# Performance work log

Hardware: AMD Instinct MI355X
Metric: run time of the kernel (lower is better)

Reference implementation:

```python
import jax, jax.numpy as jnp
import numpy as np

N = 2048          # num nodes
C = 256           # dense_dim per input
EMB = 3 * C       # 768
H = 8             # num_heads
D = EMB // H      # 96 head_dim
ALPHA = 0.2       # leaky relu slope
SCALE = D ** -0.5


def setup_inputs() -> dict:
    key = jax.random.key(0)
    ks = jax.random.split(key, 9)
    sd = EMB ** -0.5
    return {
        "eh": jax.random.normal(ks[0], (N, C), jnp.float32),
        "er": jax.random.normal(ks[1], (N, C), jnp.float32),
        "et": jax.random.normal(ks[2], (N, C), jnp.float32),
        "h_id": jax.random.randint(ks[3], (N,), 0, 32),
        "W_w": jax.random.normal(ks[4], (EMB, EMB), jnp.float32) * sd,
        "a": jax.random.normal(ks[5], (2 * D, 1), jnp.float32) * (2 * D) ** -0.5,
        "proj_w": jax.random.normal(ks[6], (EMB, EMB), jnp.float32) * sd,
        "proj_b": jnp.zeros((EMB,), jnp.float32),
        "skip_w": jax.random.normal(ks[7], (EMB, EMB), jnp.float32) * sd,
        "skip_b": jnp.zeros((EMB,), jnp.float32),
    }


def reference(eh, er, et, h_id, W_w, a, proj_w, proj_b, skip_w, skip_b):
    n = eh.shape[0]
    e = jnp.concatenate([eh, er, et], axis=-1)            # [N, EMB]
    Wh = (e @ W_w.T).reshape(n, H, D)                     # [N, H, D]

    # score = leakyrelu(a1 . Wh_scrambled[i] + a2 . Wh[j]) * scale
    a1, a2 = a[:D, 0], a[D:, 0]
    s1 = Wh @ a1                                          # [N, H]
    s2 = Wh @ a2                                          # [N, H]
    # torch's Wh.repeat(1,1,N).view(N*N,H,D) reads head (j*H + h)//N for pair (i,j,h)
    qidx = (jnp.arange(n)[:, None] * H + jnp.arange(H)[None, :]) // n  # [N, H]
    x = s1[:, qidx] + s2[None, :, :]                      # [N, N, H]
    e_ij = jnp.where(x >= 0, x, ALPHA * x) * SCALE

    mask = h_id[:, None] != h_id[None, :]                 # [N, N]
    e_ij = jnp.where(mask[:, :, None], -jnp.inf, e_ij)
    attn = jax.nn.softmax(e_ij, axis=1)                   # softmax over neighbors j

    out = jnp.einsum('ijh,jhd->ihd', attn, Wh).reshape(n, H * D)
    out = out @ proj_w.T + proj_b                         # [N, EMB]
    skip = e @ skip_w.T + skip_b                          # [N, EMB]
    return skip + out
```

## Files before the change

kernel.cpp:

```cpp
#include <hip/hip_runtime.h>
#include <hip/hip_bf16.h>

#define N_NODES 2048
#define EMB 768
#define NH 8
#define DH 96
#define ALPHA 0.2f
#define SCALE 0.10206207261596575f
#define NGMAX 192
#define WSZ (EMB * EMB)

typedef __bf16 bf16x8 __attribute__((ext_vector_type(8)));
typedef float f32x4 __attribute__((ext_vector_type(4)));
typedef __attribute__((address_space(3))) unsigned int lds_u32;
typedef __attribute__((address_space(1))) const unsigned int glb_u32;

union pack4 { ushort4 u; __hip_bfloat16 h[4]; };

__global__ __launch_bounds__(256) void prep_kernel(
    const float* __restrict__ eh, const float* __restrict__ er, const float* __restrict__ et,
    const float* __restrict__ W0, const float* __restrict__ W1, const float* __restrict__ W2,
    __hip_bfloat16* __restrict__ e, __hip_bfloat16* __restrict__ o0,
    __hip_bfloat16* __restrict__ o1, __hip_bfloat16* __restrict__ o2, int* __restrict__ cnt)
{
    const int b = blockIdx.x;
    const int gtid = b * 256 + threadIdx.x;
    if (gtid < 32) cnt[gtid] = 0;
    const float* src;
    __hip_bfloat16* dst;
    if (b < 1536) {
        int idx = gtid * 4;
        int i = idx / EMB, c = idx % EMB;
        if (c < 256)      src = eh + i * 256 + c;
        else if (c < 512) src = er + i * 256 + (c - 256);
        else              src = et + i * 256 + (c - 512);
        dst = e + (size_t)i * EMB + c;
    } else {
        int idx = (gtid - 1536 * 256) * 4;
        if (idx < WSZ)          { src = W0 + idx;           dst = o0 + idx; }
        else if (idx < 2 * WSZ) { src = W1 + idx - WSZ;     dst = o1 + idx - WSZ; }
        else                    { src = W2 + idx - 2 * WSZ; dst = o2 + idx - 2 * WSZ; }
    }
    float4 v = *reinterpret_cast<const float4*>(src);
    pack4 p;
    p.h[0] = __float2bfloat16(v.x);
    p.h[1] = __float2bfloat16(v.y);
    p.h[2] = __float2bfloat16(v.z);
    p.h[3] = __float2bfloat16(v.w);
    *reinterpret_cast<ushort4*>(dst) = p.u;
}

__device__ __forceinline__ void stage128(
    const __hip_bfloat16* __restrict__ src, int row0, int k0,
    __hip_bfloat16* lds, int wave, int lane)
{
#pragma unroll
    for (int i = 0; i < 4; i++) {
        const int c0 = wave * 256 + i * 64;
        const int c = c0 + lane;
        const int row = c >> 4;
        const int cb = (c & 15) ^ (row & 15);
        const __hip_bfloat16* g = src + (size_t)(row0 + row) * EMB + k0 + cb * 8;
        __builtin_amdgcn_global_load_lds((glb_u32*)g, (lds_u32*)(lds + c0 * 8), 16, 0, 0);
    }
}

__global__ __launch_bounds__(256) void gemm_nt_kernel(
    const __hip_bfloat16* __restrict__ A1, const __hip_bfloat16* __restrict__ B1, int ns1,
    const __hip_bfloat16* __restrict__ A2, const __hip_bfloat16* __restrict__ B2, int ns2,
    const float* __restrict__ bias1, const float* __restrict__ bias2,
    float* __restrict__ Cf)
{
    __shared__ __attribute__((aligned(16))) __hip_bfloat16 sm[2][2][8192];

    const int t = threadIdx.x;
    const int lane = t & 63, wave = t >> 6;
    const int wm = wave >> 1, wn = wave & 1;
    const int bm = blockIdx.y * 64, bn = blockIdx.x * 64;
    const int l15 = lane & 15, quad = lane >> 4;
    const int NS = ns1 + ns2;
    const int rA = wm * 32 + l15, rB = wn * 32 + l15;

    f32x4 acc00 = {0.f,0.f,0.f,0.f}, acc01 = {0.f,0.f,0.f,0.f};
    f32x4 acc10 = {0.f,0.f,0.f,0.f}, acc11 = {0.f,0.f,0.f,0.f};

    stage128(A1, bm, 0, &sm[0][0][0], wave, lane);
    stage128(B1, bn, 0, &sm[0][1][0], wave, lane);

    for (int s = 0; s < NS; s++) {
        __syncthreads();
        if (s + 1 < NS) {
            const int sn = s + 1;
            const __hip_bfloat16* As = (sn < ns1) ? A1 : A2;
            const __hip_bfloat16* Bs = (sn < ns1) ? B1 : B2;
            const int k0 = ((sn < ns1) ? sn : sn - ns1) * 128;
            stage128(As, bm, k0, &sm[sn & 1][0][0], wave, lane);
            stage128(Bs, bn, k0, &sm[sn & 1][1][0], wave, lane);
        }
        const __hip_bfloat16* At = &sm[s & 1][0][0];
        const __hip_bfloat16* Bt = &sm[s & 1][1][0];
#pragma unroll
        for (int ks = 0; ks < 4; ks++) {
            const int cq = ks * 4 + quad;
            bf16x8 a0 = *(const bf16x8*)(At + (size_t)(rA * 16        + (cq ^ l15)) * 8);
            bf16x8 a1 = *(const bf16x8*)(At + (size_t)((rA + 16) * 16 + (cq ^ l15)) * 8);
            bf16x8 b0 = *(const bf16x8*)(Bt + (size_t)(rB * 16        + (cq ^ l15)) * 8);
            bf16x8 b1 = *(const bf16x8*)(Bt + (size_t)((rB + 16) * 16 + (cq ^ l15)) * 8);
            acc00 = __builtin_amdgcn_mfma_f32_16x16x32_bf16(a0, b0, acc00, 0, 0, 0);
            acc01 = __builtin_amdgcn_mfma_f32_16x16x32_bf16(a0, b1, acc01, 0, 0, 0);
            acc10 = __builtin_amdgcn_mfma_f32_16x16x32_bf16(a1, b0, acc10, 0, 0, 0);
            acc11 = __builtin_amdgcn_mfma_f32_16x16x32_bf16(a1, b1, acc11, 0, 0, 0);
        }
    }

    const int col0 = bn + wn * 32 + l15;
    const int col1 = col0 + 16;
    float bv0 = 0.f, bv1 = 0.f;
    if (bias1 != nullptr) {
        bv0 = bias1[col0] + bias2[col0];
        bv1 = bias1[col1] + bias2[col1];
    }
    const int r0 = bm + wm * 32 + quad * 4;
#pragma unroll
    for (int r = 0; r < 4; r++) {
        const int row0 = r0 + r, row1 = r0 + 16 + r;
        Cf[(size_t)row0 * EMB + col0] = acc00[r] + bv0;
        Cf[(size_t)row0 * EMB + col1] = acc01[r] + bv1;
        Cf[(size_t)row1 * EMB + col0] = acc10[r] + bv0;
        Cf[(size_t)row1 * EMB + col1] = acc11[r] + bv1;
    }
}

__global__ __launch_bounds__(256) void s12g_kernel(
    const float* __restrict__ Wh, const float* __restrict__ a,
    float* __restrict__ s1, float* __restrict__ s2,
    const int* __restrict__ h_id, int* __restrict__ cnt, int* __restrict__ lists)
{
    int gid = blockIdx.x * 256 + threadIdx.x;
    if (gid < N_NODES) {
        int g = h_id[gid];
        int p = atomicAdd(&cnt[g], 1);
        lists[g * N_NODES + p] = gid;
    }
    int i = gid >> 3, h = gid & 7;
    const float* wr = Wh + (size_t)i * EMB + h * DH;
    float acc1 = 0.f, acc2 = 0.f;
    for (int d = 0; d < DH; d++) {
        float w = wr[d];
        acc1 += w * a[d];
        acc2 += w * a[DH + d];
    }
    s1[gid] = acc1;
    s2[gid] = acc2;
}

__global__ __launch_bounds__(256) void attn_kernel(
    const float* __restrict__ Wh, const float* __restrict__ s1, const float* __restrict__ s2,
    const int* __restrict__ cnt, const int* __restrict__ lists,
    __hip_bfloat16* __restrict__ out)
{
    const int g  = blockIdx.x & 31;
    const int h  = (blockIdx.x >> 5) & 7;
    const int dh = blockIdx.x >> 8;
    const int t  = threadIdx.x;

    __shared__ int   jb[NGMAX];
    __shared__ int   qg[NGMAX];
    __shared__ float s2g[NGMAX];
    __shared__ float s1g[NGMAX][9];
    __shared__ float Whg[NGMAX][48];

    const int ng = min(cnt[g], NGMAX);
    const int* gl = lists + g * N_NODES;

    for (int j = t; j < ng; j += 256) {
        int node = gl[j];
        jb[j]  = node;
        qg[j]  = node >> 8;
        s2g[j] = s2[node * 8 + h];
        float4 v0 = *reinterpret_cast<const float4*>(s1 + node * 8);
        float4 v1 = *reinterpret_cast<const float4*>(s1 + node * 8 + 4);
        s1g[j][0] = v0.x; s1g[j][1] = v0.y; s1g[j][2] = v0.z; s1g[j][3] = v0.w;
        s1g[j][4] = v1.x; s1g[j][5] = v1.y; s1g[j][6] = v1.z; s1g[j][7] = v1.w;
    }
    __syncthreads();
    for (int idx = t; idx < ng * 12; idx += 256) {
        int jc = idx / 12, dq = idx % 12;
        float4 v = *reinterpret_cast<const float4*>(
            Wh + (size_t)jb[jc] * EMB + h * DH + dh * 48 + dq * 4);
        *reinterpret_cast<float4*>(&Whg[jc][dq * 4]) = v;
    }
    __syncthreads();

    if (t < ng) {
        float m = -1e30f;
        for (int j = 0; j < ng; j++) {
            float x = s1g[t][qg[j]] + s2g[j];
            float ev = (x >= 0.f ? x : ALPHA * x) * SCALE;
            m = fmaxf(m, ev);
        }
        float S = 0.f;
        for (int j = 0; j < ng; j++) {
            float x = s1g[t][qg[j]] + s2g[j];
            float ev = (x >= 0.f ? x : ALPHA * x) * SCALE;
            S += __expf(ev - m);
        }
        const float ri = 1.f / S;

        float acc[48];
#pragma unroll
        for (int d = 0; d < 48; d++) acc[d] = 0.f;
        for (int j = 0; j < ng; j++) {
            float x = s1g[t][qg[j]] + s2g[j];
            float ev = (x >= 0.f ? x : ALPHA * x) * SCALE;
            float p = __expf(ev - m) * ri;
#pragma unroll
            for (int d = 0; d < 48; d++) acc[d] += p * Whg[j][d];
        }
        __hip_bfloat16* po = out + (size_t)jb[t] * EMB + h * DH + dh * 48;
#pragma unroll
        for (int d = 0; d < 48; d += 4) {
            pack4 pk;
            pk.h[0] = __float2bfloat16(acc[d]);
            pk.h[1] = __float2bfloat16(acc[d + 1]);
            pk.h[2] = __float2bfloat16(acc[d + 2]);
            pk.h[3] = __float2bfloat16(acc[d + 3]);
            *reinterpret_cast<ushort4*>(po + d) = pk.u;
        }
    }
}

extern "C" void kernel_launch(void* const* d_in, const int* in_sizes, int n_in,
                              void* d_out, int out_size, void* d_ws, size_t ws_size,
                              hipStream_t stream)
{
    const float* eh     = (const float*)d_in[0];
    const float* er     = (const float*)d_in[1];
    const float* et     = (const float*)d_in[2];
    const int*   h_id   = (const int*)d_in[3];
    const float* W_w    = (const float*)d_in[4];
    const float* a      = (const float*)d_in[5];
    const float* proj_w = (const float*)d_in[6];
    const float* proj_b = (const float*)d_in[7];
    const float* skip_w = (const float*)d_in[8];
    const float* skip_b = (const float*)d_in[9];
    float* out = (float*)d_out;

    char* ws = (char*)d_ws;
    __hip_bfloat16* e_ws   = (__hip_bfloat16*)(ws);
    float*          Wh_ws  = (float*)(ws + 3145728);
    __hip_bfloat16* at_ws  = (__hip_bfloat16*)(ws + 9437184);
    __hip_bfloat16* Wb_ws  = (__hip_bfloat16*)(ws + 12582912);
    __hip_bfloat16* Pb_ws  = (__hip_bfloat16*)(ws + 13762560);
    __hip_bfloat16* Sb_ws  = (__hip_bfloat16*)(ws + 14942208);
    float*          s1_ws  = (float*)(ws + 16121856);
    float*          s2_ws  = (float*)(ws + 16187392);
    int*            cnt_ws = (int*)(ws + 16252928);
    int*            lst_ws = (int*)(ws + 16253056);

    prep_kernel<<<3264, 256, 0, stream>>>(eh, er, et, W_w, proj_w, skip_w,
                                          e_ws, Wb_ws, Pb_ws, Sb_ws, cnt_ws);

    gemm_nt_kernel<<<dim3(12, 32), 256, 0, stream>>>(
        e_ws, Wb_ws, 6, nullptr, nullptr, 0, nullptr, nullptr, Wh_ws);

    s12g_kernel<<<64, 256, 0, stream>>>(Wh_ws, a, s1_ws, s2_ws, h_id, cnt_ws, lst_ws);

    attn_kernel<<<512, 256, 0, stream>>>(Wh_ws, s1_ws, s2_ws, cnt_ws, lst_ws, at_ws);

    gemm_nt_kernel<<<dim3(12, 32), 256, 0, stream>>>(
        at_ws, Pb_ws, 6, e_ws, Sb_ws, 6, proj_b, skip_b, out);
}
```

Before: 135.6 us.

## Split-K GEMMs with atomic accumulation, fuse score dot-products, deterministic group lists

```diff
diff --git a/kernel.cpp b/kernel.cpp
--- a/kernel.cpp
+++ b/kernel.cpp
@@ -20,46 +20,69 @@
 __global__ __launch_bounds__(256) void prep_kernel(
     const float* __restrict__ eh, const float* __restrict__ er, const float* __restrict__ et,
     const float* __restrict__ W0, const float* __restrict__ W1, const float* __restrict__ W2,
+    const int* __restrict__ h_id,
     __hip_bfloat16* __restrict__ e, __hip_bfloat16* __restrict__ o0,
-    __hip_bfloat16* __restrict__ o1, __hip_bfloat16* __restrict__ o2, int* __restrict__ cnt)
+    __hip_bfloat16* __restrict__ o1, __hip_bfloat16* __restrict__ o2,
+    float4* __restrict__ zbase, int* __restrict__ cnt, int* __restrict__ lists)
 {
     const int b = blockIdx.x;
-    const int gtid = b * 256 + threadIdx.x;
-    if (gtid < 32) cnt[gtid] = 0;
-    const float* src;
-    __hip_bfloat16* dst;
-    if (b < 1536) {
-        int idx = gtid * 4;
-        int i = idx / EMB, c = idx % EMB;
-        if (c < 256)      src = eh + i * 256 + c;
-        else if (c < 512) src = er + i * 256 + (c - 256);
-        else              src = et + i * 256 + (c - 512);
-        dst = e + (size_t)i * EMB + c;
+    const int t = threadIdx.x;
+    if (b < 3264) {
+        const int gtid = b * 256 + t;
+        const float* src;
+        __hip_bfloat16* dst;
+        if (b < 1536) {
+            int idx = gtid * 4;
+            int i = idx / EMB, c = idx % EMB;
+            if (c < 256)      src = eh + i * 256 + c;
+            else if (c < 512) src = er + i * 256 + (c - 256);
+            else              src = et + i * 256 + (c - 512);
+            dst = e + (size_t)i * EMB + c;
+        } else {
+            int idx = (gtid - 1536 * 256) * 4;
+            if (idx < WSZ)          { src = W0 + idx;           dst = o0 + idx; }
+            else if (idx < 2 * WSZ) { src = W1 + idx - WSZ;     dst = o1 + idx - WSZ; }
+            else                    { src = W2 + idx - 2 * WSZ; dst = o2 + idx - 2 * WSZ; }
+        }
+        float4 v = *reinterpret_cast<const float4*>(src);
+        pack4 p;
+        p.h[0] = __float2bfloat16(v.x);
+        p.h[1] = __float2bfloat16(v.y);
+        p.h[2] = __float2bfloat16(v.z);
+        p.h[3] = __float2bfloat16(v.w);
+        *reinterpret_cast<ushort4*>(dst) = p.u;
+    } else if (b < 4832) {
+        const float4 z = {0.f, 0.f, 0.f, 0.f};
+        zbase[(size_t)(b - 3264) * 256 + t] = z;
     } else {
-        int idx = (gtid - 1536 * 256) * 4;
-        if (idx < WSZ)          { src = W0 + idx;           dst = o0 + idx; }
-        else if (idx < 2 * WSZ) { src = W1 + idx - WSZ;     dst = o1 + idx - WSZ; }
-        else                    { src = W2 + idx - 2 * WSZ; dst = o2 + idx - 2 * WSZ; }
-    }
-    float4 v = *reinterpret_cast<const float4*>(src);
-    pack4 p;
-    p.h[0] = __float2bfloat16(v.x);
-    p.h[1] = __float2bfloat16(v.y);
-    p.h[2] = __float2bfloat16(v.z);
-    p.h[3] = __float2bfloat16(v.w);
-    *reinterpret_cast<ushort4*>(dst) = p.u;
-}
-
-__device__ __forceinline__ void stage128(
+        __shared__ int hh[N_NODES];
+        __shared__ int seg[32][8];
+        for (int j = t; j < N_NODES; j += 256) hh[j] = h_id[j];
+        __syncthreads();
+        const int g = t >> 3, s = t & 7;
+        int c = 0;
+        for (int j = s * 256; j < s * 256 + 256; j++) c += (hh[j] == g) ? 1 : 0;
+        seg[g][s] = c;
+        __syncthreads();
+        int off = 0;
+        for (int k = 0; k < s; k++) off += seg[g][k];
+        int p = off;
+        for (int j = s * 256; j < s * 256 + 256; j++)
+            if (hh[j] == g) lists[g * N_NODES + (p++)] = j;
+        if (s == 7) cnt[g] = off + c;
+    }
+}
+
+__device__ __forceinline__ void stage64(
     const __hip_bfloat16* __restrict__ src, int row0, int k0,
     __hip_bfloat16* lds, int wave, int lane)
 {
 #pragma unroll
-    for (int i = 0; i < 4; i++) {
-        const int c0 = wave * 256 + i * 64;
+    for (int i = 0; i < 2; i++) {
+        const int c0 = wave * 128 + i * 64;
         const int c = c0 + lane;
-        const int row = c >> 4;
-        const int cb = (c & 15) ^ (row & 15);
+        const int row = c >> 3;
+        const int cb = (c & 7) ^ (row & 7);
         const __hip_bfloat16* g = src + (size_t)(row0 + row) * EMB + k0 + cb * 8;
         __builtin_amdgcn_global_load_lds((glb_u32*)g, (lds_u32*)(lds + c0 * 8), 16, 0, 0);
     }
@@ -69,14 +92,16 @@
     const __hip_bfloat16* __restrict__ A1, const __hip_bfloat16* __restrict__ B1, int ns1,
     const __hip_bfloat16* __restrict__ A2, const __hip_bfloat16* __restrict__ B2, int ns2,
     const float* __restrict__ bias1, const float* __restrict__ bias2,
+    const float* __restrict__ avec, float* __restrict__ s1, float* __restrict__ s2,
     float* __restrict__ Cf)
 {
-    __shared__ __attribute__((aligned(16))) __hip_bfloat16 sm[2][2][8192];
+    __shared__ __attribute__((aligned(16))) __hip_bfloat16 sm[2][2][4096];
 
     const int t = threadIdx.x;
     const int lane = t & 63, wave = t >> 6;
     const int wm = wave >> 1, wn = wave & 1;
     const int bm = blockIdx.y * 64, bn = blockIdx.x * 64;
+    const int kbase = blockIdx.z * (ns1 * 64);
     const int l15 = lane & 15, quad = lane >> 4;
     const int NS = ns1 + ns2;
     const int rA = wm * 32 + l15, rB = wn * 32 + l15;
@@ -84,8 +109,8 @@
     f32x4 acc00 = {0.f,0.f,0.f,0.f}, acc01 = {0.f,0.f,0.f,0.f};
     f32x4 acc10 = {0.f,0.f,0.f,0.f}, acc11 = {0.f,0.f,0.f,0.f};
 
-    stage128(A1, bm, 0, &sm[0][0][0], wave, lane);
-    stage128(B1, bn, 0, &sm[0][1][0], wave, lane);
+    stage64(A1, bm, kbase, &sm[0][0][0], wave, lane);
+    stage64(B1, bn, kbase, &sm[0][1][0], wave, lane);
 
     for (int s = 0; s < NS; s++) {
         __syncthreads();
@@ -93,19 +118,19 @@
             const int sn = s + 1;
             const __hip_bfloat16* As = (sn < ns1) ? A1 : A2;
             const __hip_bfloat16* Bs = (sn < ns1) ? B1 : B2;
-            const int k0 = ((sn < ns1) ? sn : sn - ns1) * 128;
-            stage128(As, bm, k0, &sm[sn & 1][0][0], wave, lane);
-            stage128(Bs, bn, k0, &sm[sn & 1][1][0], wave, lane);
+            const int k0 = kbase + ((sn < ns1) ? sn : sn - ns1) * 64;
+            stage64(As, bm, k0, &sm[sn & 1][0][0], wave, lane);
+            stage64(Bs, bn, k0, &sm[sn & 1][1][0], wave, lane);
         }
         const __hip_bfloat16* At = &sm[s & 1][0][0];
         const __hip_bfloat16* Bt = &sm[s & 1][1][0];
 #pragma unroll
-        for (int ks = 0; ks < 4; ks++) {
+        for (int ks = 0; ks < 2; ks++) {
             const int cq = ks * 4 + quad;
-            bf16x8 a0 = *(const bf16x8*)(At + (size_t)(rA * 16        + (cq ^ l15)) * 8);
-            bf16x8 a1 = *(const bf16x8*)(At + (size_t)((rA + 16) * 16 + (cq ^ l15)) * 8);
-            bf16x8 b0 = *(const bf16x8*)(Bt + (size_t)(rB * 16        + (cq ^ l15)) * 8);
-            bf16x8 b1 = *(const bf16x8*)(Bt + (size_t)((rB + 16) * 16 + (cq ^ l15)) * 8);
+            bf16x8 a0 = *(const bf16x8*)(At + (size_t)(rA * 8        + (cq ^ (rA & 7))) * 8);
+            bf16x8 a1 = *(const bf16x8*)(At + (size_t)((rA + 16) * 8 + (cq ^ (rA & 7))) * 8);
+            bf16x8 b0 = *(const bf16x8*)(Bt + (size_t)(rB * 8        + (cq ^ (rB & 7))) * 8);
+            bf16x8 b1 = *(const bf16x8*)(Bt + (size_t)((rB + 16) * 8 + (cq ^ (rB & 7))) * 8);
             acc00 = __builtin_amdgcn_mfma_f32_16x16x32_bf16(a0, b0, acc00, 0, 0, 0);
             acc01 = __builtin_amdgcn_mfma_f32_16x16x32_bf16(a0, b1, acc01, 0, 0, 0);
             acc10 = __builtin_amdgcn_mfma_f32_16x16x32_bf16(a1, b0, acc10, 0, 0, 0);
@@ -116,7 +141,7 @@
     const int col0 = bn + wn * 32 + l15;
     const int col1 = col0 + 16;
     float bv0 = 0.f, bv1 = 0.f;
-    if (bias1 != nullptr) {
+    if (bias1 != nullptr && blockIdx.z == 0) {
         bv0 = bias1[col0] + bias2[col0];
         bv1 = bias1[col1] + bias2[col1];
     }
@@ -124,45 +149,56 @@
 #pragma unroll
     for (int r = 0; r < 4; r++) {
         const int row0 = r0 + r, row1 = r0 + 16 + r;
-        Cf[(size_t)row0 * EMB + col0] = acc00[r] + bv0;
-        Cf[(size_t)row0 * EMB + col1] = acc01[r] + bv1;
-        Cf[(size_t)row1 * EMB + col0] = acc10[r] + bv0;
-        Cf[(size_t)row1 * EMB + col1] = acc11[r] + bv1;
-    }
-}
-
-__global__ __launch_bounds__(256) void s12g_kernel(
-    const float* __restrict__ Wh, const float* __restrict__ a,
-    float* __restrict__ s1, float* __restrict__ s2,
-    const int* __restrict__ h_id, int* __restrict__ cnt, int* __restrict__ lists)
-{
-    int gid = blockIdx.x * 256 + threadIdx.x;
-    if (gid < N_NODES) {
-        int g = h_id[gid];
-        int p = atomicAdd(&cnt[g], 1);
-        lists[g * N_NODES + p] = gid;
-    }
-    int i = gid >> 3, h = gid & 7;
-    const float* wr = Wh + (size_t)i * EMB + h * DH;
-    float acc1 = 0.f, acc2 = 0.f;
-    for (int d = 0; d < DH; d++) {
-        float w = wr[d];
-        acc1 += w * a[d];
-        acc2 += w * a[DH + d];
-    }
-    s1[gid] = acc1;
-    s2[gid] = acc2;
+        atomicAdd(&Cf[(size_t)row0 * EMB + col0], acc00[r] + bv0);
+        atomicAdd(&Cf[(size_t)row0 * EMB + col1], acc01[r] + bv1);
+        atomicAdd(&Cf[(size_t)row1 * EMB + col0], acc10[r] + bv0);
+        atomicAdd(&Cf[(size_t)row1 * EMB + col1], acc11[r] + bv1);
+    }
+
+    if (avec != nullptr) {
+        const int cb0 = bn + wn * 32;
+        const int h = cb0 / DH;
+        const int ch = cb0 % DH + l15;
+        const float a10 = avec[ch],      a11 = avec[ch + 16];
+        const float a20 = avec[DH + ch], a21 = avec[DH + ch + 16];
+#pragma unroll
+        for (int r = 0; r < 4; r++) {
+            float v1a = acc00[r] * a10 + acc01[r] * a11;
+            float v2a = acc00[r] * a20 + acc01[r] * a21;
+            float v1b = acc10[r] * a10 + acc11[r] * a11;
+            float v2b = acc10[r] * a20 + acc11[r] * a21;
+#pragma unroll
+            for (int m = 1; m < 16; m <<= 1) {
+                v1a += __shfl_xor(v1a, m);
+                v2a += __shfl_xor(v2a, m);
+                v1b += __shfl_xor(v1b, m);
+                v2b += __shfl_xor(v2b, m);
+            }
+            if (l15 == 0) {
+                atomicAdd(&s1[(r0 + r) * NH + h], v1a);
+                atomicAdd(&s2[(r0 + r) * NH + h], v2a);
+                atomicAdd(&s1[(r0 + 16 + r) * NH + h], v1b);
+                atomicAdd(&s2[(r0 + 16 + r) * NH + h], v2b);
+            }
+        }
+    }
 }
 
 __global__ __launch_bounds__(256) void attn_kernel(
     const float* __restrict__ Wh, const float* __restrict__ s1, const float* __restrict__ s2,
     const int* __restrict__ cnt, const int* __restrict__ lists,
-    __hip_bfloat16* __restrict__ out)
+    __hip_bfloat16* __restrict__ out, float4* __restrict__ outz)
 {
     const int g  = blockIdx.x & 31;
     const int h  = (blockIdx.x >> 5) & 7;
     const int dh = blockIdx.x >> 8;
     const int t  = threadIdx.x;
+
+    {
+        const float4 z = {0.f, 0.f, 0.f, 0.f};
+        const int zb = blockIdx.x * 768 + t;
+        outz[zb] = z; outz[zb + 256] = z; outz[zb + 512] = z;
+    }
 
     __shared__ int   jb[NGMAX];
     __shared__ int   qg[NGMAX];
@@ -192,34 +228,36 @@
     }
     __syncthreads();
 
-    if (t < ng) {
+    const int half = t >> 7;
+    const int d0 = half * 24;
+    for (int tr = t & 127; tr < ng; tr += 128) {
         float m = -1e30f;
         for (int j = 0; j < ng; j++) {
-            float x = s1g[t][qg[j]] + s2g[j];
+            float x = s1g[tr][qg[j]] + s2g[j];
             float ev = (x >= 0.f ? x : ALPHA * x) * SCALE;
             m = fmaxf(m, ev);
         }
         float S = 0.f;
         for (int j = 0; j < ng; j++) {
-            float x = s1g[t][qg[j]] + s2g[j];
+            float x = s1g[tr][qg[j]] + s2g[j];
             float ev = (x >= 0.f ? x : ALPHA * x) * SCALE;
             S += __expf(ev - m);
         }
         const float ri = 1.f / S;
 
-        float acc[48];
-#pragma unroll
-        for (int d = 0; d < 48; d++) acc[d] = 0.f;
+        float acc[24];
+#pragma unroll
+        for (int d = 0; d < 24; d++) acc[d] = 0.f;
         for (int j = 0; j < ng; j++) {
-            float x = s1g[t][qg[j]] + s2g[j];
+            float x = s1g[tr][qg[j]] + s2g[j];
             float ev = (x >= 0.f ? x : ALPHA * x) * SCALE;
             float p = __expf(ev - m) * ri;
 #pragma unroll
-            for (int d = 0; d < 48; d++) acc[d] += p * Whg[j][d];
-        }
-        __hip_bfloat16* po = out + (size_t)jb[t] * EMB + h * DH + dh * 48;
-#pragma unroll
-        for (int d = 0; d < 48; d += 4) {
+            for (int d = 0; d < 24; d++) acc[d] += p * Whg[j][d0 + d];
+        }
+        __hip_bfloat16* po = out + (size_t)jb[tr] * EMB + h * DH + dh * 48 + d0;
+#pragma unroll
+        for (int d = 0; d < 24; d += 4) {
             pack4 pk;
             pk.h[0] = __float2bfloat16(acc[d]);
             pk.h[1] = __float2bfloat16(acc[d + 1]);
@@ -249,25 +287,27 @@
     char* ws = (char*)d_ws;
     __hip_bfloat16* e_ws   = (__hip_bfloat16*)(ws);
     float*          Wh_ws  = (float*)(ws + 3145728);
-    __hip_bfloat16* at_ws  = (__hip_bfloat16*)(ws + 9437184);
-    __hip_bfloat16* Wb_ws  = (__hip_bfloat16*)(ws + 12582912);
-    __hip_bfloat16* Pb_ws  = (__hip_bfloat16*)(ws + 13762560);
-    __hip_bfloat16* Sb_ws  = (__hip_bfloat16*)(ws + 14942208);
-    float*          s1_ws  = (float*)(ws + 16121856);
-    float*          s2_ws  = (float*)(ws + 16187392);
-    int*            cnt_ws = (int*)(ws + 16252928);
-    int*            lst_ws = (int*)(ws + 16253056);
-
-    prep_kernel<<<3264, 256, 0, stream>>>(eh, er, et, W_w, proj_w, skip_w,
-                                          e_ws, Wb_ws, Pb_ws, Sb_ws, cnt_ws);
-
-    gemm_nt_kernel<<<dim3(12, 32), 256, 0, stream>>>(
-        e_ws, Wb_ws, 6, nullptr, nullptr, 0, nullptr, nullptr, Wh_ws);
-
-    s12g_kernel<<<64, 256, 0, stream>>>(Wh_ws, a, s1_ws, s2_ws, h_id, cnt_ws, lst_ws);
-
-    attn_kernel<<<512, 256, 0, stream>>>(Wh_ws, s1_ws, s2_ws, cnt_ws, lst_ws, at_ws);
-
-    gemm_nt_kernel<<<dim3(12, 32), 256, 0, stream>>>(
-        at_ws, Pb_ws, 6, e_ws, Sb_ws, 6, proj_b, skip_b, out);
-}
+    float*          s1_ws  = (float*)(ws + 9437184);
+    float*          s2_ws  = (float*)(ws + 9502720);
+    __hip_bfloat16* at_ws  = (__hip_bfloat16*)(ws + 9568256);
+    __hip_bfloat16* Wb_ws  = (__hip_bfloat16*)(ws + 12713984);
+    __hip_bfloat16* Pb_ws  = (__hip_bfloat16*)(ws + 13893632);
+    __hip_bfloat16* Sb_ws  = (__hip_bfloat16*)(ws + 15073280);
+    int*            lst_ws = (int*)(ws + 16252928);
+    int*            cnt_ws = (int*)(ws + 16515072);
+
+    prep_kernel<<<4833, 256, 0, stream>>>(eh, er, et, W_w, proj_w, skip_w, h_id,
+                                          e_ws, Wb_ws, Pb_ws, Sb_ws,
+                                          (float4*)(ws + 3145728), cnt_ws, lst_ws);
+
+    gemm_nt_kernel<<<dim3(12, 32, 2), 256, 0, stream>>>(
+        e_ws, Wb_ws, 6, nullptr, nullptr, 0, nullptr, nullptr,
+        a, s1_ws, s2_ws, Wh_ws);
+
+    attn_kernel<<<512, 256, 0, stream>>>(Wh_ws, s1_ws, s2_ws, cnt_ws, lst_ws,
+                                         at_ws, (float4*)out);
+
+    gemm_nt_kernel<<<dim3(12, 32, 2), 256, 0, stream>>>(
+        at_ws, Pb_ws, 6, e_ws, Sb_ws, 6, proj_b, skip_b,
+        nullptr, nullptr, nullptr, out);
+}
```

Measured after the change: 168.5 us. +24.2%, slower.

## Fuse skip GEMM into Wh GEMM launch and split attention head dims across threads

Applied to the files above, without the earlier changes.

```diff
diff --git a/kernel.cpp b/kernel.cpp
--- a/kernel.cpp
+++ b/kernel.cpp
@@ -65,37 +65,40 @@
     }
 }
 
-__global__ __launch_bounds__(256) void gemm_nt_kernel(
-    const __hip_bfloat16* __restrict__ A1, const __hip_bfloat16* __restrict__ B1, int ns1,
-    const __hip_bfloat16* __restrict__ A2, const __hip_bfloat16* __restrict__ B2, int ns2,
+__global__ __launch_bounds__(256) void gemm_kernel(
+    const __hip_bfloat16* __restrict__ A,
+    const __hip_bfloat16* __restrict__ B1, const __hip_bfloat16* __restrict__ B2,
     const float* __restrict__ bias1, const float* __restrict__ bias2,
-    float* __restrict__ Cf)
+    float* __restrict__ C1, float* __restrict__ C2,
+    int nbn1, int accum)
 {
     __shared__ __attribute__((aligned(16))) __hip_bfloat16 sm[2][2][8192];
 
     const int t = threadIdx.x;
     const int lane = t & 63, wave = t >> 6;
     const int wm = wave >> 1, wn = wave & 1;
-    const int bm = blockIdx.y * 64, bn = blockIdx.x * 64;
+    const int bnb = blockIdx.x;
+    const bool second = bnb >= nbn1;
+    const __hip_bfloat16* B = second ? B2 : B1;
+    float* Cf = second ? C2 : C1;
+    const int bn = (second ? bnb - nbn1 : bnb) * 64;
+    const int bm = blockIdx.y * 64;
     const int l15 = lane & 15, quad = lane >> 4;
-    const int NS = ns1 + ns2;
     const int rA = wm * 32 + l15, rB = wn * 32 + l15;
 
     f32x4 acc00 = {0.f,0.f,0.f,0.f}, acc01 = {0.f,0.f,0.f,0.f};
     f32x4 acc10 = {0.f,0.f,0.f,0.f}, acc11 = {0.f,0.f,0.f,0.f};
 
-    stage128(A1, bm, 0, &sm[0][0][0], wave, lane);
-    stage128(B1, bn, 0, &sm[0][1][0], wave, lane);
-
-    for (int s = 0; s < NS; s++) {
+    stage128(A, bm, 0, &sm[0][0][0], wave, lane);
+    stage128(B, bn, 0, &sm[0][1][0], wave, lane);
+
+#pragma unroll 1
+    for (int s = 0; s < 6; s++) {
         __syncthreads();
-        if (s + 1 < NS) {
-            const int sn = s + 1;
-            const __hip_bfloat16* As = (sn < ns1) ? A1 : A2;
-            const __hip_bfloat16* Bs = (sn < ns1) ? B1 : B2;
-            const int k0 = ((sn < ns1) ? sn : sn - ns1) * 128;
-            stage128(As, bm, k0, &sm[sn & 1][0][0], wave, lane);
-            stage128(Bs, bn, k0, &sm[sn & 1][1][0], wave, lane);
+        if (s + 1 < 6) {
+            const int k0 = (s + 1) * 128;
+            stage128(A, bm, k0, &sm[(s + 1) & 1][0][0], wave, lane);
+            stage128(B, bn, k0, &sm[(s + 1) & 1][1][0], wave, lane);
         }
         const __hip_bfloat16* At = &sm[s & 1][0][0];
         const __hip_bfloat16* Bt = &sm[s & 1][1][0];
@@ -116,7 +119,7 @@
     const int col0 = bn + wn * 32 + l15;
     const int col1 = col0 + 16;
     float bv0 = 0.f, bv1 = 0.f;
-    if (bias1 != nullptr) {
+    if (second && bias1 != nullptr) {
         bv0 = bias1[col0] + bias2[col0];
         bv1 = bias1[col1] + bias2[col1];
     }
@@ -124,10 +127,21 @@
 #pragma unroll
     for (int r = 0; r < 4; r++) {
         const int row0 = r0 + r, row1 = r0 + 16 + r;
-        Cf[(size_t)row0 * EMB + col0] = acc00[r] + bv0;
-        Cf[(size_t)row0 * EMB + col1] = acc01[r] + bv1;
-        Cf[(size_t)row1 * EMB + col0] = acc10[r] + bv0;
-        Cf[(size_t)row1 * EMB + col1] = acc11[r] + bv1;
+        float* p00 = &Cf[(size_t)row0 * EMB + col0];
+        float* p01 = &Cf[(size_t)row0 * EMB + col1];
+        float* p10 = &Cf[(size_t)row1 * EMB + col0];
+        float* p11 = &Cf[(size_t)row1 * EMB + col1];
+        if (accum) {
+            *p00 += acc00[r];
+            *p01 += acc01[r];
+            *p10 += acc10[r];
+            *p11 += acc11[r];
+        } else {
+            *p00 = acc00[r] + bv0;
+            *p01 = acc01[r] + bv1;
+            *p10 = acc10[r] + bv0;
+            *p11 = acc11[r] + bv1;
+        }
     }
 }
 
@@ -192,34 +206,36 @@
     }
     __syncthreads();
 
-    if (t < ng) {
+    const int half = t >> 7;
+    const int d0 = half * 24;
+    for (int tr = t & 127; tr < ng; tr += 128) {
         float m = -1e30f;
         for (int j = 0; j < ng; j++) {
-            float x = s1g[t][qg[j]] + s2g[j];
+            float x = s1g[tr][qg[j]] + s2g[j];
             float ev = (x >= 0.f ? x : ALPHA * x) * SCALE;
             m = fmaxf(m, ev);
         }
         float S = 0.f;
         for (int j = 0; j < ng; j++) {
-            float x = s1g[t][qg[j]] + s2g[j];
+            float x = s1g[tr][qg[j]] + s2g[j];
             float ev = (x >= 0.f ? x : ALPHA * x) * SCALE;
             S += __expf(ev - m);
         }
         const float ri = 1.f / S;
 
-        float acc[48];
-#pragma unroll
-        for (int d = 0; d < 48; d++) acc[d] = 0.f;
+        float acc[24];
+#pragma unroll
+        for (int d = 0; d < 24; d++) acc[d] = 0.f;
         for (int j = 0; j < ng; j++) {
-            float x = s1g[t][qg[j]] + s2g[j];
+            float x = s1g[tr][qg[j]] + s2g[j];
             float ev = (x >= 0.f ? x : ALPHA * x) * SCALE;
             float p = __expf(ev - m) * ri;
 #pragma unroll
-            for (int d = 0; d < 48; d++) acc[d] += p * Whg[j][d];
-        }
-        __hip_bfloat16* po = out + (size_t)jb[t] * EMB + h * DH + dh * 48;
-#pragma unroll
-        for (int d = 0; d < 48; d += 4) {
+            for (int d = 0; d < 24; d++) acc[d] += p * Whg[j][d0 + d];
+        }
+        __hip_bfloat16* po = out + (size_t)jb[tr] * EMB + h * DH + dh * 48 + d0;
+#pragma unroll
+        for (int d = 0; d < 24; d += 4) {
             pack4 pk;
             pk.h[0] = __float2bfloat16(acc[d]);
             pk.h[1] = __float2bfloat16(acc[d + 1]);
@@ -261,13 +277,13 @@
     prep_kernel<<<3264, 256, 0, stream>>>(eh, er, et, W_w, proj_w, skip_w,
                                           e_ws, Wb_ws, Pb_ws, Sb_ws, cnt_ws);
 
-    gemm_nt_kernel<<<dim3(12, 32), 256, 0, stream>>>(
-        e_ws, Wb_ws, 6, nullptr, nullptr, 0, nullptr, nullptr, Wh_ws);
+    gemm_kernel<<<dim3(24, 32), 256, 0, stream>>>(
+        e_ws, Wb_ws, Sb_ws, proj_b, skip_b, Wh_ws, out, 12, 0);
 
     s12g_kernel<<<64, 256, 0, stream>>>(Wh_ws, a, s1_ws, s2_ws, h_id, cnt_ws, lst_ws);
 
     attn_kernel<<<512, 256, 0, stream>>>(Wh_ws, s1_ws, s2_ws, cnt_ws, lst_ws, at_ws);
 
-    gemm_nt_kernel<<<dim3(12, 32), 256, 0, stream>>>(
-        at_ws, Pb_ws, 6, e_ws, Sb_ws, 6, proj_b, skip_b, out);
-}
+    gemm_kernel<<<dim3(12, 32), 256, 0, stream>>>(
+        at_ws, Pb_ws, nullptr, nullptr, nullptr, out, nullptr, 12, 1);
+}
```

Result: no change. 134.2 us (median of 2 runs) (-1.1%).
